# Optimization experiments

Hardware: AMD Instinct MI355X
Metric: run time of the kernel (lower is better)

Reference implementation:

```python
import jax, jax.numpy as jnp
import numpy as np

DIM = 256
NUM_HEADS = 8
STRIPE_W = 2
HEAD_DIM = DIM // NUM_HEADS


def setup_inputs() -> dict:
    key = jax.random.key(0)
    ks = jax.random.split(key, 3)
    B, H, W = 8, 128, 128
    s = 0.02
    return {
        "x": jax.random.normal(ks[0], (B, H, W, DIM), jnp.float32),
        "Wqkv": jax.random.normal(ks[1], (DIM, 3 * DIM), jnp.float32) * s,
        "bqkv": jnp.zeros((3 * DIM,), jnp.float32),
        "Wproj": jax.random.normal(ks[2], (DIM, DIM), jnp.float32) * s,
        "bproj": jnp.zeros((DIM,), jnp.float32),
        "gamma": jnp.ones((DIM,), jnp.float32),
        "beta": jnp.zeros((DIM,), jnp.float32),
    }


def _layernorm(x, g, b, eps=1e-5):
    m = jnp.mean(x, axis=-1, keepdims=True)
    v = jnp.mean(jnp.square(x - m), axis=-1, keepdims=True)
    return (x - m) * jax.lax.rsqrt(v + eps) * g + b


def _stripe_attn(xn, Wqkv, bqkv, horizontal):
    # horizontal: stripes along H; vertical: transpose spatial dims first
    if not horizontal:
        xn = xn.transpose(0, 2, 1, 3)
    B, A, L, C = xn.shape  # A = stripe axis, L = in-stripe axis
    hh = NUM_HEADS // 2
    hd = hh * HEAD_DIM
    off = 0 if horizontal else hd  # first half of heads -> horizontal, second -> vertical
    qkv = xn @ Wqkv + bqkv
    q = qkv[..., off:off + hd]
    k = qkv[..., C + off:C + off + hd]
    v = qkv[..., 2 * C + off:2 * C + off + hd]
    ns = max(1, A // STRIPE_W)
    sw = A // ns

    def r(t):  # (B, A, L, hd) -> (B*ns, hh, sw*L, head_dim)
        return (t[:, :ns * sw]
                .reshape(B, ns, sw, L, hh, HEAD_DIM)
                .transpose(0, 1, 4, 2, 3, 5)
                .reshape(B * ns, hh, sw * L, HEAD_DIM))

    q, k, v = r(q), r(k), r(v)
    scale = HEAD_DIM ** (-0.5)
    attn = jax.nn.softmax(jnp.einsum('bhqd,bhkd->bhqk', q, k) * scale, axis=-1)
    out = jnp.einsum('bhqk,bhkd->bhqd', attn, v)
    out = (out.reshape(B, ns, hh, sw, L, HEAD_DIM)
           .transpose(0, 1, 3, 4, 2, 5)
           .reshape(B, ns * sw, L, hd))
    if ns * sw < A:
        out = jnp.pad(out, ((0, 0), (0, A - ns * sw), (0, 0), (0, 0)))
    if not horizontal:
        out = out.transpose(0, 2, 1, 3)
    return out


def reference(x, Wqkv, bqkv, Wproj, bproj, gamma, beta):
    xn = _layernorm(x, gamma, beta)
    h = jnp.concatenate([
        _stripe_attn(xn, Wqkv, bqkv, True),
        _stripe_attn(xn, Wqkv, bqkv, False),
    ], axis=-1)
    return h @ Wproj + bproj + x
```

## Files before the change

kernel.cpp:

```cpp
#include <hip/hip_runtime.h>
#include <hip/hip_bf16.h>

typedef __hip_bfloat16 bf16;
typedef unsigned short u16;
typedef unsigned int u32;
typedef __attribute__((ext_vector_type(8))) short short8;
typedef __attribute__((ext_vector_type(4))) float floatx4;

#define NROWS (8*128*128)
#define DIM 256
#define QKVN 768
#define HD 32
#define SEQ 256

__device__ __forceinline__ float b2f_bits(u16 u) {
    union { float f; u32 i; } x; x.i = ((u32)u) << 16; return x.f;
}
__device__ __forceinline__ u16 f2b_bits(float f) {
    bf16 h = __float2bfloat16(f);
    return *reinterpret_cast<u16*>(&h);
}
__device__ __forceinline__ u32 pack2(float a, float b) {
    return ((u32)f2b_bits(b) << 16) | (u32)f2b_bits(a);
}
__device__ __forceinline__ void load8f(const bf16* p, float* d) {
    uint4 w = *reinterpret_cast<const uint4*>(p);
    d[0] = b2f_bits((u16)(w.x & 0xffff)); d[1] = b2f_bits((u16)(w.x >> 16));
    d[2] = b2f_bits((u16)(w.y & 0xffff)); d[3] = b2f_bits((u16)(w.y >> 16));
    d[4] = b2f_bits((u16)(w.z & 0xffff)); d[5] = b2f_bits((u16)(w.z >> 16));
    d[6] = b2f_bits((u16)(w.w & 0xffff)); d[7] = b2f_bits((u16)(w.w >> 16));
}
__device__ __forceinline__ void gload16(const void* g, void* l) {
    __builtin_amdgcn_global_load_lds(
        (const __attribute__((address_space(1))) void*)g,
        (__attribute__((address_space(3))) void*)l, 16, 0, 0);
}

__global__ __launch_bounds__(256) void convert_kernel(
        const float* __restrict__ Wqkv, const float* __restrict__ Wproj,
        bf16* __restrict__ WTq, bf16* __restrict__ WTp) {
    const int n = blockIdx.x;
    const int k = threadIdx.x;
    if (n < QKVN) {
        WTq[(size_t)n * DIM + k] = __float2bfloat16(Wqkv[(size_t)k * QKVN + n]);
    } else {
        const int n2 = n - QKVN;
        WTp[(size_t)n2 * DIM + k] = __float2bfloat16(Wproj[(size_t)k * DIM + n2]);
    }
}

__global__ __launch_bounds__(256) void ln_kernel(
        const float* __restrict__ x, const float* __restrict__ gamma,
        const float* __restrict__ beta, bf16* __restrict__ xn,
        size_t x_off, int nrows) {
    const int t = threadIdx.x;
    const int wv = t >> 6, lane = t & 63;
    const int nwaves = gridDim.x << 2;
    const int wid = (blockIdx.x << 2) + wv;

    const float4 g4 = *reinterpret_cast<const float4*>(gamma + lane * 4);
    const float4 b4 = *reinterpret_cast<const float4*>(beta + lane * 4);

    for (int row = wid; row < nrows; row += nwaves) {
        const float4 v = *reinterpret_cast<const float4*>(
            x + x_off + (size_t)row * DIM + lane * 4);

        float s = v.x + v.y + v.z + v.w;
        #pragma unroll
        for (int off = 32; off > 0; off >>= 1) s += __shfl_xor(s, off, 64);
        const float mean = s * (1.0f / DIM);

        const float dx = v.x - mean, dy = v.y - mean;
        const float dz = v.z - mean, dw = v.w - mean;
        float s2 = dx * dx + dy * dy + dz * dz + dw * dw;
        #pragma unroll
        for (int off = 32; off > 0; off >>= 1) s2 += __shfl_xor(s2, off, 64);
        const float rstd = rsqrtf(s2 * (1.0f / DIM) + 1e-5f);

        uint2 o;
        o.x = pack2(dx * rstd * g4.x + b4.x, dy * rstd * g4.y + b4.y);
        o.y = pack2(dz * rstd * g4.z + b4.z, dw * rstd * g4.w + b4.w);
        *reinterpret_cast<uint2*>(xn + (size_t)row * DIM + lane * 4) = o;
    }
}

template<int OUT_F32>
__global__ __launch_bounds__(256) void gemm_mfma(
        const bf16* __restrict__ A, const bf16* __restrict__ WT,
        const float* __restrict__ bias, const float* __restrict__ resid,
        void* __restrict__ Cout, int N) {
    __shared__ __align__(16) bf16 As[128][32];
    __shared__ __align__(16) bf16 Bs[128][32];

    const int tid = threadIdx.x;
    const int lane = tid & 63, wave = tid >> 6;
    const int wm = (wave >> 1) * 64, wn = (wave & 1) * 64;
    const int m = lane & 15, quad = lane >> 4;

    const int nwg = gridDim.x * gridDim.y;
    const int L = blockIdx.y * gridDim.x + blockIdx.x;
    const int tile = (L & 7) * (nwg >> 3) + (L >> 3);
    const int bx = tile % gridDim.x, by = tile / gridDim.x;
    const int row0 = by * 128, col0 = bx * 128;

    floatx4 acc[4][4] = {};

    const int c0 = tid, c1 = tid + 256;
    const int r0_ = c0 >> 2, o0 = (c0 & 3) * 8;
    const int r1_ = c1 >> 2, o1 = (c1 & 3) * 8;

    for (int k0 = 0; k0 < DIM; k0 += 32) {
        __syncthreads();
        gload16(A  + (size_t)(row0 + r0_) * DIM + k0 + o0, (bf16*)As + c0 * 8);
        gload16(A  + (size_t)(row0 + r1_) * DIM + k0 + o1, (bf16*)As + c1 * 8);
        gload16(WT + (size_t)(col0 + r0_) * DIM + k0 + o0, (bf16*)Bs + c0 * 8);
        gload16(WT + (size_t)(col0 + r1_) * DIM + k0 + o1, (bf16*)Bs + c1 * 8);
        __syncthreads();

        short8 af[4], bfr[4];
        #pragma unroll
        for (int i = 0; i < 4; i++)
            af[i] = *reinterpret_cast<const short8*>(&As[wm + i * 16 + m][quad * 8]);
        #pragma unroll
        for (int j = 0; j < 4; j++)
            bfr[j] = *reinterpret_cast<const short8*>(&Bs[wn + j * 16 + m][quad * 8]);
        #pragma unroll
        for (int i = 0; i < 4; i++) {
            #pragma unroll
            for (int j = 0; j < 4; j++) {
                if constexpr (OUT_F32) {
                    acc[i][j] = __builtin_amdgcn_mfma_f32_16x16x32_bf16(
                        af[i], bfr[j], acc[i][j], 0, 0, 0);
                } else {
                    acc[i][j] = __builtin_amdgcn_mfma_f32_16x16x32_bf16(
                        bfr[j], af[i], acc[i][j], 0, 0, 0);
                }
            }
        }
    }

    if constexpr (OUT_F32) {
        #pragma unroll
        for (int j = 0; j < 4; j++) {
            const int col = col0 + wn + j * 16 + m;
            const float bj = bias[col];
            #pragma unroll
            for (int i = 0; i < 4; i++) {
                #pragma unroll
                for (int r = 0; r < 4; r++) {
                    const int row = row0 + wm + i * 16 + quad * 4 + r;
                    ((float*)Cout)[(size_t)row * N + col] =
                        acc[i][j][r] + bj + resid[(size_t)row * N + col];
                }
            }
        }
    } else {
        __shared__ __align__(16) u16 Cs[4][64][64];
        #pragma unroll
        for (int i = 0; i < 4; i++) {
            const int rr = i * 16 + m;
            const int sx = (m & 7) << 3;
            #pragma unroll
            for (int j = 0; j < 4; j++) {
                const int cc = j * 16 + quad * 4;
                const float4 bj = *reinterpret_cast<const float4*>(
                    &bias[col0 + wn + cc]);
                u32* p = reinterpret_cast<u32*>(&Cs[wave][rr][cc ^ sx]);
                p[0] = pack2(acc[i][j][0] + bj.x, acc[i][j][1] + bj.y);
                p[1] = pack2(acc[i][j][2] + bj.z, acc[i][j][3] + bj.w);
            }
        }
        #pragma unroll
        for (int p = 0; p < 8; p++) {
            const int rr = p * 8 + (lane >> 3);
            const int cc = (lane & 7) * 8;
            const uint4 v = *reinterpret_cast<const uint4*>(
                &Cs[wave][rr][cc ^ ((rr & 7) << 3)]);
            *reinterpret_cast<uint4*>(
                &((bf16*)Cout)[(size_t)(row0 + wm + rr) * N + col0 + wn + cc]) = v;
        }
    }
}

__global__ __launch_bounds__(256) void attn_kernel(
        const bf16* __restrict__ qkv, bf16* __restrict__ h) {
    __shared__ __align__(16) u16 Ks[SEQ][HD];
    __shared__ __align__(16) u16 Vt[HD][264];
    __shared__ __align__(16) u16 Ps[4][64][40];

    const int bid = blockIdx.x;
    const int head = bid & 3;
    const int s = (bid >> 2) & 63;
    const int dir = bid >> 8;
    const int b = blockIdx.y;

    const int t = threadIdx.x;
    const int w = t >> 6, lane = t & 63;
    const int m = lane & 15, quad = lane >> 4;
    const int qoff = dir * 128 + head * HD;

    auto row_of = [&](int idx) -> size_t {
        const int al = idx >> 7, l = idx & 127;
        int hp, wp;
        if (dir == 0) { hp = 2 * s + al; wp = l; }
        else          { wp = 2 * s + al; hp = l; }
        return ((size_t)(b * 128 + hp)) * 128 + wp;
    };

    #pragma unroll
    for (int j = 0; j < 4; j++) {
        const int e = t * 8 + j * 2048;
        const int key = e >> 5;
        const int ko = e & 31;
        gload16(qkv + row_of(key) * QKVN + 256 + qoff + ko, (u16*)Ks + e);
    }

    {
        const bf16* vp = qkv + row_of(t) * QKVN + 512 + qoff;
        const uint4 v0 = *reinterpret_cast<const uint4*>(vp);
        const uint4 v1 = *reinterpret_cast<const uint4*>(vp + 8);
        const uint4 v2 = *reinterpret_cast<const uint4*>(vp + 16);
        const uint4 v3 = *reinterpret_cast<const uint4*>(vp + 24);
        const u32 ww[16] = { v0.x, v0.y, v0.z, v0.w, v1.x, v1.y, v1.z, v1.w,
                             v2.x, v2.y, v2.z, v2.w, v3.x, v3.y, v3.z, v3.w };
        #pragma unroll
        for (int d = 0; d < 16; d++) {
            Vt[2 * d][t]     = (u16)(ww[d] & 0xffff);
            Vt[2 * d + 1][t] = (u16)(ww[d] >> 16);
        }
    }

    short8 qf[4];
    #pragma unroll
    for (int i = 0; i < 4; i++)
        qf[i] = *reinterpret_cast<const short8*>(
            qkv + row_of(w * 64 + i * 16 + m) * QKVN + qoff + quad * 8);

    __syncthreads();

    const float scale = 0.17677669529663687f;
    floatx4 acc[4][2] = {};
    floatx4 rs[4] = {};

    for (int c = 0; c < 8; c++) {
        const short8 kf0 = *reinterpret_cast<const short8*>(&Ks[c * 32 + m][quad * 8]);
        const short8 kf1 = *reinterpret_cast<const short8*>(&Ks[c * 32 + 16 + m][quad * 8]);

        #pragma unroll
        for (int i = 0; i < 4; i++) {
            const floatx4 z = {};
            floatx4 s0 = __builtin_amdgcn_mfma_f32_16x16x32_bf16(qf[i], kf0, z, 0, 0, 0);
            floatx4 s1 = __builtin_amdgcn_mfma_f32_16x16x32_bf16(qf[i], kf1, z, 0, 0, 0);
            #pragma unroll
            for (int r = 0; r < 4; r++) {
                const float p0 = __expf(s0[r] * scale);
                const float p1 = __expf(s1[r] * scale);
                rs[i][r] += p0 + p1;
                Ps[w][i * 16 + quad * 4 + r][m]      = f2b_bits(p0);
                Ps[w][i * 16 + quad * 4 + r][16 + m] = f2b_bits(p1);
            }
        }
        __syncthreads();

        const short8 vf0 = *reinterpret_cast<const short8*>(&Vt[m][c * 32 + quad * 8]);
        const short8 vf1 = *reinterpret_cast<const short8*>(&Vt[16 + m][c * 32 + quad * 8]);

        #pragma unroll
        for (int i = 0; i < 4; i++) {
            const short8 pf = *reinterpret_cast<const short8*>(&Ps[w][i * 16 + m][quad * 8]);
            acc[i][0] = __builtin_amdgcn_mfma_f32_16x16x32_bf16(pf, vf0, acc[i][0], 0, 0, 0);
            acc[i][1] = __builtin_amdgcn_mfma_f32_16x16x32_bf16(pf, vf1, acc[i][1], 0, 0, 0);
        }
        __syncthreads();
    }

    #pragma unroll
    for (int i = 0; i < 4; i++) {
        #pragma unroll
        for (int r = 0; r < 4; r++) {
            float v = rs[i][r];
            v += __shfl_xor(v, 1);
            v += __shfl_xor(v, 2);
            v += __shfl_xor(v, 4);
            v += __shfl_xor(v, 8);
            rs[i][r] = v;
        }
    }

    #pragma unroll
    for (int i = 0; i < 4; i++) {
        #pragma unroll
        for (int r = 0; r < 4; r++) {
            const float inv = 1.0f / rs[i][r];
            bf16* op = h + row_of(w * 64 + i * 16 + quad * 4 + r) * DIM + qoff;
            op[m]      = __float2bfloat16(acc[i][0][r] * inv);
            op[16 + m] = __float2bfloat16(acc[i][1][r] * inv);
        }
    }
}

extern "C" void kernel_launch(void* const* d_in, const int* in_sizes, int n_in,
                              void* d_out, int out_size, void* d_ws, size_t ws_size,
                              hipStream_t stream) {
    const float* x     = (const float*)d_in[0];
    const float* Wqkv  = (const float*)d_in[1];
    const float* bqkv  = (const float*)d_in[2];
    const float* Wproj = (const float*)d_in[3];
    const float* bproj = (const float*)d_in[4];
    const float* gamma = (const float*)d_in[5];
    const float* beta  = (const float*)d_in[6];
    char* ws = (char*)d_ws;

    const size_t MB256 = (size_t)268435456;
    if (ws_size >= MB256 + 524288) {
        bf16* xn_h = (bf16*)ws;
        bf16* qkv  = (bf16*)(ws + (size_t)NROWS * DIM * 2);
        bf16* WTq  = (bf16*)(ws + MB256);
        bf16* WTp  = WTq + (size_t)QKVN * DIM;

        convert_kernel<<<QKVN + DIM, 256, 0, stream>>>(Wqkv, Wproj, WTq, WTp);
        ln_kernel<<<2048, 256, 0, stream>>>(x, gamma, beta, xn_h, 0, NROWS);
        gemm_mfma<0><<<dim3(QKVN / 128, NROWS / 128), 256, 0, stream>>>(
            xn_h, WTq, bqkv, nullptr, qkv, QKVN);
        attn_kernel<<<dim3(512, 8), 256, 0, stream>>>(qkv, xn_h);
        gemm_mfma<1><<<dim3(DIM / 128, NROWS / 128), 256, 0, stream>>>(
            xn_h, WTp, bproj, x, d_out, DIM);
    } else {
        const int MB = NROWS / 8;
        bf16* WTq   = (bf16*)ws;
        bf16* WTp   = WTq + (size_t)QKVN * DIM;
        bf16* xn_b  = (bf16*)(ws + (size_t)1048576);
        bf16* qkv_b = (bf16*)(ws + (size_t)9 * 1048576);
        bf16* h_b   = (bf16*)(ws + (size_t)33 * 1048576);

        convert_kernel<<<QKVN + DIM, 256, 0, stream>>>(Wqkv, Wproj, WTq, WTp);
        for (int b = 0; b < 8; b++) {
            const size_t ro = (size_t)b * MB * DIM;
            ln_kernel<<<2048, 256, 0, stream>>>(x, gamma, beta, xn_b, ro, MB);
            gemm_mfma<0><<<dim3(QKVN / 128, MB / 128), 256, 0, stream>>>(
                xn_b, WTq, bqkv, nullptr, qkv_b, QKVN);
            attn_kernel<<<dim3(512, 1), 256, 0, stream>>>(qkv_b, h_b);
            gemm_mfma<1><<<dim3(DIM / 128, MB / 128), 256, 0, stream>>>(
                h_b, WTp, bproj, x + ro, (float*)d_out + ro, DIM);
        }
    }
}
```

Measured before the change: 518.8 us.

## Transpose score MFMA, pack P stores, drop block barriers in stripe attention

Swaps the MFMA operands so each lane holds contiguous key scores for one query. This lets probabilities be packed into 64-bit LDS stores and row sums be reduced with fewer shuffles. Uses exp2 with a folded log2e scale, removes the two per-chunk __syncthreads since each wave uses a private P buffer, and raises wave priority around the PV MFMAs. Correctness relies on per-wave ordering of the LDS writes and reads of P.

```diff
diff --git a/kernel.cpp b/kernel.cpp
--- a/kernel.cpp
+++ b/kernel.cpp
@@ -238,9 +238,9 @@
 
     __syncthreads();
 
-    const float scale = 0.17677669529663687f;
+    const float C = 0.25503494f;
     floatx4 acc[4][2] = {};
-    floatx4 rs[4] = {};
+    float rsl[4] = {};
 
     for (int c = 0; c < 8; c++) {
         const short8 kf0 = *reinterpret_cast<const short8*>(&Ks[c * 32 + m][quad * 8]);
@@ -249,18 +249,21 @@
         #pragma unroll
         for (int i = 0; i < 4; i++) {
             const floatx4 z = {};
-            floatx4 s0 = __builtin_amdgcn_mfma_f32_16x16x32_bf16(qf[i], kf0, z, 0, 0, 0);
-            floatx4 s1 = __builtin_amdgcn_mfma_f32_16x16x32_bf16(qf[i], kf1, z, 0, 0, 0);
+            floatx4 s0 = __builtin_amdgcn_mfma_f32_16x16x32_bf16(kf0, qf[i], z, 0, 0, 0);
+            floatx4 s1 = __builtin_amdgcn_mfma_f32_16x16x32_bf16(kf1, qf[i], z, 0, 0, 0);
+            float p0[4], p1[4];
             #pragma unroll
             for (int r = 0; r < 4; r++) {
-                const float p0 = __expf(s0[r] * scale);
-                const float p1 = __expf(s1[r] * scale);
-                rs[i][r] += p0 + p1;
-                Ps[w][i * 16 + quad * 4 + r][m]      = f2b_bits(p0);
-                Ps[w][i * 16 + quad * 4 + r][16 + m] = f2b_bits(p1);
+                p0[r] = exp2f(s0[r] * C);
+                p1[r] = exp2f(s1[r] * C);
+                rsl[i] += p0[r] + p1[r];
             }
-        }
-        __syncthreads();
+            uint2 wa, wb;
+            wa.x = pack2(p0[0], p0[1]); wa.y = pack2(p0[2], p0[3]);
+            wb.x = pack2(p1[0], p1[1]); wb.y = pack2(p1[2], p1[3]);
+            *reinterpret_cast<uint2*>(&Ps[w][i * 16 + m][4 * quad])      = wa;
+            *reinterpret_cast<uint2*>(&Ps[w][i * 16 + m][16 + 4 * quad]) = wb;
+        }
 
         const short8 vf0 = *reinterpret_cast<const short8*>(&Vt[m][c * 32 + quad * 8]);
         const short8 vf1 = *reinterpret_cast<const short8*>(&Vt[16 + m][c * 32 + quad * 8]);
@@ -268,30 +271,22 @@
         #pragma unroll
         for (int i = 0; i < 4; i++) {
             const short8 pf = *reinterpret_cast<const short8*>(&Ps[w][i * 16 + m][quad * 8]);
+            __builtin_amdgcn_s_setprio(1);
             acc[i][0] = __builtin_amdgcn_mfma_f32_16x16x32_bf16(pf, vf0, acc[i][0], 0, 0, 0);
             acc[i][1] = __builtin_amdgcn_mfma_f32_16x16x32_bf16(pf, vf1, acc[i][1], 0, 0, 0);
-        }
-        __syncthreads();
+            __builtin_amdgcn_s_setprio(0);
+        }
     }
 
     #pragma unroll
     for (int i = 0; i < 4; i++) {
+        float v = rsl[i];
+        v += __shfl_xor(v, 16, 64);
+        v += __shfl_xor(v, 32, 64);
         #pragma unroll
         for (int r = 0; r < 4; r++) {
-            float v = rs[i][r];
-            v += __shfl_xor(v, 1);
-            v += __shfl_xor(v, 2);
-            v += __shfl_xor(v, 4);
-            v += __shfl_xor(v, 8);
-            rs[i][r] = v;
-        }
-    }
-
-    #pragma unroll
-    for (int i = 0; i < 4; i++) {
-        #pragma unroll
-        for (int r = 0; r < 4; r++) {
-            const float inv = 1.0f / rs[i][r];
+            const float rv = __shfl(v, quad * 4 + r, 64);
+            const float inv = 1.0f / rv;
             bf16* op = h + row_of(w * 64 + i * 16 + quad * 4 + r) * DIM + qoff;
             op[m]      = __float2bfloat16(acc[i][0][r] * inv);
             op[16 + m] = __float2bfloat16(acc[i][1][r] * inv);
```

New measurement: 543.1 us. 4.7% more time.
